# Kernel optimization log

Measured on AMD Instinct MI355X. Metric: run time of the kernel, lower is better.

## Reference

```python
import jax, jax.numpy as jnp
import numpy as np

N, E, F_IN, NUM_GRAPHS, K = 50000, 500000, 160, 128, 3


def _glorot(k, shape):
    lim = np.sqrt(6.0 / (shape[-2] + shape[-1])).astype(np.float32)
    return jax.random.uniform(k, shape, jnp.float32, -lim, lim)


def setup_inputs() -> dict:
    key = jax.random.key(0)
    ks = jax.random.split(key, 8)
    x = jax.random.normal(ks[0], (N, F_IN), jnp.float32)
    edge_index = jax.random.randint(ks[1], (2, E), 0, N)
    edge_attr = jax.random.uniform(ks[2], (E,), jnp.float32)
    batch = jnp.sort(jax.random.randint(ks[3], (N,), 0, NUM_GRAPHS))
    W1 = _glorot(ks[4], (K, F_IN, 128)); b1 = jnp.zeros((128,), jnp.float32)
    W2 = _glorot(ks[5], (K, 128, 64)); b2 = jnp.zeros((64,), jnp.float32)
    W3 = _glorot(ks[6], (K, 64, 32)); b3 = jnp.zeros((32,), jnp.float32)
    Wl = _glorot(ks[7], (32, 2)); bl = jnp.zeros((2,), jnp.float32)
    return dict(x=x, edge_index=edge_index, edge_attr=edge_attr, batch=batch,
                W1=W1, b1=b1, W2=W2, b2=b2, W3=W3, b3=b3, Wl=Wl, bl=bl)


def _cheb_norm(src, dst, edge_attr, n):
    # PyG ChebConv: sym-normalized Laplacian, lambda_max=2 =>
    # L_hat = (2/lmax)*L_sym - I = -D^{-1/2} A D^{-1/2} (diagonal = 0)
    deg = jax.ops.segment_sum(edge_attr, src, num_segments=n)
    safe = jnp.where(deg > 0, deg, 1.0)
    dinv = jnp.where(deg > 0, jax.lax.rsqrt(safe), 0.0)
    return -dinv[src] * edge_attr * dinv[dst]


def _propagate(x, src, dst, w, n):
    # out[dst] += w * x[src]  (sparse L_hat @ x)
    return jax.ops.segment_sum(w[:, None] * x[src], dst, num_segments=n)


def _cheb_conv(x, src, dst, w, W, b, n):
    # Chebyshev recurrence: T0 = x, T1 = L_hat x, Tk = 2 L_hat T(k-1) - T(k-2)
    tx0 = x
    out = tx0 @ W[0]
    tx1 = _propagate(tx0, src, dst, w, n)
    out = out + tx1 @ W[1]
    for k in range(2, W.shape[0]):
        tx2 = 2.0 * _propagate(tx1, src, dst, w, n) - tx0
        out = out + tx2 @ W[k]
        tx0, tx1 = tx1, tx2
    return out + b


def reference(x, edge_index, edge_attr, batch, W1, b1, W2, b2, W3, b3, Wl, bl):
    n = x.shape[0]
    src, dst = edge_index[0], edge_index[1]
    w = _cheb_norm(src, dst, edge_attr, n)
    h = jax.nn.relu(_cheb_conv(x, src, dst, w, W1, b1, n))
    h = jax.nn.relu(_cheb_conv(h, src, dst, w, W2, b2, n))
    h = jax.nn.relu(_cheb_conv(h, src, dst, w, W3, b3, n))
    # global_mean_pool over graph ids (dropout omitted: eval mode)
    sums = jax.ops.segment_sum(h, batch, num_segments=NUM_GRAPHS)
    cnt = jax.ops.segment_sum(jnp.ones((n,), h.dtype), batch, num_segments=NUM_GRAPHS)
    pooled = sums / jnp.maximum(cnt, 1.0)[:, None]
    return pooled @ Wl + bl
```

## Files before the change

kernel.cpp:

```cpp
#include <hip/hip_runtime.h>

#define N_NODES 50000
#define N_EDGES 500000
#define NUM_G   128
#define SCAN_NB 49
#define SCAN_PAD (SCAN_NB * 1024)

typedef __attribute__((ext_vector_type(8))) short short8;
typedef __attribute__((ext_vector_type(4))) float f32x4;

__device__ __forceinline__ unsigned f2bf(float x) {
    unsigned u = __float_as_uint(x);
    return (u + 0x7FFFu + ((u >> 16) & 1u)) >> 16;
}
__device__ __forceinline__ float bf2f(unsigned h) {
    return __uint_as_float(h << 16);
}

__global__ void deg_count_kernel(const int* __restrict__ src, const int* __restrict__ dst,
                                 const float* __restrict__ ea,
                                 float* __restrict__ deg, int* __restrict__ cnt, int E) {
    int e = blockIdx.x * blockDim.x + threadIdx.x;
    if (e < E) {
        atomicAdd(&deg[src[e]], ea[e]);
        atomicAdd(&cnt[dst[e]], 1);
    }
}

__global__ void dinv_kernel(const float* __restrict__ deg, float* __restrict__ dinv, int n) {
    int i = blockIdx.x * blockDim.x + threadIdx.x;
    if (i >= n) return;
    float d = deg[i];
    float r = 0.0f;
    if (d > 0.0f) {
        r = rsqrtf(d);
        r = r * (1.5f - 0.5f * d * r * r);
    }
    dinv[i] = r;
}

__global__ void scan_partial_kernel(const int* __restrict__ cnt, int* __restrict__ partial) {
    int b = blockIdx.x, t = threadIdx.x;
    int4 v = reinterpret_cast<const int4*>(cnt)[b * 256 + t];
    int s = v.x + v.y + v.z + v.w;
    __shared__ int red[256];
    red[t] = s;
    __syncthreads();
    for (int off = 128; off > 0; off >>= 1) {
        if (t < off) red[t] += red[t + off];
        __syncthreads();
    }
    if (t == 0) partial[b] = red[0];
}

__global__ void scan_offsets_kernel(int* __restrict__ partial, int* __restrict__ rowptr,
                                    int nb, int n) {
    int t = threadIdx.x;
    int orig = (t < nb) ? partial[t] : 0;
    int v = orig;
    for (int off = 1; off < 64; off <<= 1) {
        int u = __shfl_up(v, off, 64);
        if (t >= off) v += u;
    }
    if (t < nb) partial[t] = v - orig;
    if (t == nb - 1) rowptr[n] = v;
}

__global__ void scan_final_kernel(const int* __restrict__ cnt, const int* __restrict__ partial,
                                  int* __restrict__ rowptr, int n) {
    int b = blockIdx.x, t = threadIdx.x;
    int4 v = reinterpret_cast<const int4*>(cnt)[b * 256 + t];
    int s = v.x + v.y + v.z + v.w;
    __shared__ int red[256];
    red[t] = s;
    __syncthreads();
    for (int off = 1; off < 256; off <<= 1) {
        int u = (t >= off) ? red[t - off] : 0;
        __syncthreads();
        red[t] += u;
        __syncthreads();
    }
    int excl = partial[b] + ((t == 0) ? 0 : red[t - 1]);
    int i0 = b * 1024 + t * 4;
    if (i0 < n)     rowptr[i0]     = excl;
    if (i0 + 1 < n) rowptr[i0 + 1] = excl + v.x;
    if (i0 + 2 < n) rowptr[i0 + 2] = excl + v.x + v.y;
    if (i0 + 3 < n) rowptr[i0 + 3] = excl + v.x + v.y + v.z;
}

__global__ void scatter_kernel(const int* __restrict__ src, const int* __restrict__ dst,
                               const float* __restrict__ ea, const float* __restrict__ dinv,
                               const int* __restrict__ rowptr, int* __restrict__ fill,
                               int* __restrict__ csr_src, float* __restrict__ csr_w, int E) {
    int e = blockIdx.x * blockDim.x + threadIdx.x;
    if (e >= E) return;
    int s = src[e], d = dst[e];
    float wv = -dinv[s] * ea[e] * dinv[d];
    int pos = rowptr[d] + atomicAdd(&fill[d], 1);
    csr_src[pos] = s;
    csr_w[pos] = wv;
}

__global__ void conv_bf16_kernel(const float* __restrict__ x, unsigned short* __restrict__ o, int n4) {
    int t = blockIdx.x * blockDim.x + threadIdx.x;
    if (t >= n4) return;
    float4 v = reinterpret_cast<const float4*>(x)[t];
    ushort4 r;
    r.x = (unsigned short)f2bf(v.x);
    r.y = (unsigned short)f2bf(v.y);
    r.z = (unsigned short)f2bf(v.z);
    r.w = (unsigned short)f2bf(v.w);
    *reinterpret_cast<ushort4*>(o + (size_t)t * 4) = r;
}

__global__ void wprep_kernel(const float* __restrict__ W, unsigned short* __restrict__ WT,
                             int FIN, int F) {
    int t = blockIdx.x * blockDim.x + threadIdx.x;
    int total = 3 * F * FIN;
    if (t >= total) return;
    int n = t / FIN, k = t - n * FIN;
    int sel = n / F, c = n - sel * F;
    float v;
    if (sel == 0) v = W[(size_t)k * F + c] - W[(size_t)2 * FIN * F + (size_t)k * F + c];
    else          v = W[(size_t)sel * FIN * F + (size_t)k * F + c];
    WT[t] = (unsigned short)f2bf(v);
}

template<int FIN, int F>
__launch_bounds__(256)
__global__ void cheb_gemm(const unsigned short* __restrict__ Xb, const unsigned short* __restrict__ WT,
                          unsigned short* __restrict__ Y0, unsigned short* __restrict__ Y1,
                          unsigned short* __restrict__ Y2,
                          int nrows) {
    constexpr int KT = FIN / 32;
    constexpr int NT = F / 32;
    constexpr int SA = FIN + 8;
    constexpr int F8 = FIN / 8;
    __shared__ short Bs[32 * SA];

    int tid = threadIdx.x;
    int lane = tid & 63, w = tid >> 6;
    int m0 = blockIdx.x * 64;
    int g = blockIdx.y;
    unsigned short* Ys = (g == 0) ? Y0 : (g == 1) ? Y1 : Y2;

    int colb = lane & 15;
    int q8 = (lane >> 4) << 3;
    int rq = (lane >> 4) << 2;
    int arow = m0 + w * 16 + colb;
    bool rok = arow < nrows;

    short8 afr[KT];
    #pragma unroll
    for (int kt = 0; kt < KT; ++kt) {
        short8 z = {0, 0, 0, 0, 0, 0, 0, 0};
        afr[kt] = rok ? *reinterpret_cast<const short8*>(Xb + (size_t)arow * FIN + (kt << 5) + q8) : z;
    }

    for (int nt = 0; nt < NT; ++nt) {
        int n0 = (g * NT + nt) << 5;
        __syncthreads();
        for (int span = tid; span < 32 * F8; span += 256) {
            int r = span / F8, c8 = (span - r * F8) << 3;
            int pr = (r < 16) ? (r << 1) : (((r - 16) << 1) + 1);
            *reinterpret_cast<uint4*>(&Bs[r * SA + c8]) =
                *reinterpret_cast<const uint4*>(WT + (size_t)(n0 + pr) * FIN + c8);
        }
        __syncthreads();

        f32x4 acc0 = {0.f, 0.f, 0.f, 0.f}, acc1 = acc0;
        #pragma unroll
        for (int kt = 0; kt < KT; ++kt) {
            short8 b0 = *reinterpret_cast<const short8*>(&Bs[colb * SA + (kt << 5) + q8]);
            short8 b1 = *reinterpret_cast<const short8*>(&Bs[(colb + 16) * SA + (kt << 5) + q8]);
            acc0 = __builtin_amdgcn_mfma_f32_16x16x32_bf16(afr[kt], b0, acc0, 0, 0, 0);
            acc1 = __builtin_amdgcn_mfma_f32_16x16x32_bf16(afr[kt], b1, acc1, 0, 0, 0);
        }

        int lc = (nt << 5) + (colb << 1);
        #pragma unroll
        for (int r = 0; r < 4; ++r) {
            int orow = m0 + w * 16 + rq + r;
            if (orow < nrows) {
                unsigned pack = f2bf(acc0[r]) | (f2bf(acc1[r]) << 16);
                *reinterpret_cast<unsigned*>(Ys + (size_t)orow * F + lc) = pack;
            }
        }
    }
}

__device__ __forceinline__ void acc8(float* acc, uint4 p, float wv) {
    acc[0] += wv * bf2f(p.x & 0xFFFFu);
    acc[1] += wv * __uint_as_float(p.x & 0xFFFF0000u);
    acc[2] += wv * bf2f(p.y & 0xFFFFu);
    acc[3] += wv * __uint_as_float(p.y & 0xFFFF0000u);
    acc[4] += wv * bf2f(p.z & 0xFFFFu);
    acc[5] += wv * __uint_as_float(p.z & 0xFFFF0000u);
    acc[6] += wv * bf2f(p.w & 0xFFFFu);
    acc[7] += wv * __uint_as_float(p.w & 0xFFFF0000u);
}

__device__ __forceinline__ void expand8(uint4 p, float* o) {
    o[0] = bf2f(p.x & 0xFFFFu);
    o[1] = __uint_as_float(p.x & 0xFFFF0000u);
    o[2] = bf2f(p.y & 0xFFFFu);
    o[3] = __uint_as_float(p.y & 0xFFFF0000u);
    o[4] = bf2f(p.z & 0xFFFFu);
    o[5] = __uint_as_float(p.z & 0xFFFF0000u);
    o[6] = bf2f(p.w & 0xFFFFu);
    o[7] = __uint_as_float(p.w & 0xFFFF0000u);
}

__global__ void gather_z_kernel(const unsigned short* __restrict__ X, const int* __restrict__ csr_src,
                                const float* __restrict__ csr_w, const int* __restrict__ rowptr,
                                const unsigned short* __restrict__ Y1, unsigned short* __restrict__ U,
                                int n, int F) {
    int Fq8 = F >> 3;
    int t = blockIdx.x * blockDim.x + threadIdx.x;
    int d = t / Fq8;
    if (d >= n) return;
    int f8 = (t - d * Fq8) << 3;
    int beg = rowptr[d], end = rowptr[d + 1];
    float acc[8] = {0.f, 0.f, 0.f, 0.f, 0.f, 0.f, 0.f, 0.f};
    int i = beg;
    for (; i + 1 < end; i += 2) {
        int s0 = csr_src[i], s1 = csr_src[i + 1];
        float w0 = csr_w[i], w1 = csr_w[i + 1];
        uint4 p0 = *reinterpret_cast<const uint4*>(X + (size_t)s0 * F + f8);
        uint4 p1 = *reinterpret_cast<const uint4*>(X + (size_t)s1 * F + f8);
        acc8(acc, p0, w0);
        acc8(acc, p1, w1);
    }
    if (i < end) {
        uint4 p0 = *reinterpret_cast<const uint4*>(X + (size_t)csr_src[i] * F + f8);
        acc8(acc, p0, csr_w[i]);
    }
    float y[8];
    expand8(*reinterpret_cast<const uint4*>(Y1 + (size_t)d * F + f8), y);
    uint4 o;
    o.x = f2bf(y[0] + 2.f * acc[0]) | (f2bf(y[1] + 2.f * acc[1]) << 16);
    o.y = f2bf(y[2] + 2.f * acc[2]) | (f2bf(y[3] + 2.f * acc[3]) << 16);
    o.z = f2bf(y[4] + 2.f * acc[4]) | (f2bf(y[5] + 2.f * acc[5]) << 16);
    o.w = f2bf(y[6] + 2.f * acc[6]) | (f2bf(y[7] + 2.f * acc[7]) << 16);
    *reinterpret_cast<uint4*>(U + (size_t)d * F + f8) = o;
}

__global__ void gather_v_kernel(const unsigned short* __restrict__ X, const int* __restrict__ csr_src,
                                const float* __restrict__ csr_w, const int* __restrict__ rowptr,
                                const unsigned short* __restrict__ Y0, const float* __restrict__ bias,
                                unsigned short* __restrict__ Xn, int n, int F) {
    int Fq8 = F >> 3;
    int t = blockIdx.x * blockDim.x + threadIdx.x;
    int d = t / Fq8;
    if (d >= n) return;
    int f8 = (t - d * Fq8) << 3;
    int beg = rowptr[d], end = rowptr[d + 1];
    float acc[8] = {0.f, 0.f, 0.f, 0.f, 0.f, 0.f, 0.f, 0.f};
    int i = beg;
    for (; i + 1 < end; i += 2) {
        int s0 = csr_src[i], s1 = csr_src[i + 1];
        float w0 = csr_w[i], w1 = csr_w[i + 1];
        uint4 p0 = *reinterpret_cast<const uint4*>(X + (size_t)s0 * F + f8);
        uint4 p1 = *reinterpret_cast<const uint4*>(X + (size_t)s1 * F + f8);
        acc8(acc, p0, w0);
        acc8(acc, p1, w1);
    }
    if (i < end) {
        uint4 p0 = *reinterpret_cast<const uint4*>(X + (size_t)csr_src[i] * F + f8);
        acc8(acc, p0, csr_w[i]);
    }
    float y[8];
    expand8(*reinterpret_cast<const uint4*>(Y0 + (size_t)d * F + f8), y);
    float4 ba = *reinterpret_cast<const float4*>(bias + f8);
    float4 bb = *reinterpret_cast<const float4*>(bias + f8 + 4);
    float v0 = fmaxf(y[0] + acc[0] + ba.x, 0.f);
    float v1 = fmaxf(y[1] + acc[1] + ba.y, 0.f);
    float v2 = fmaxf(y[2] + acc[2] + ba.z, 0.f);
    float v3 = fmaxf(y[3] + acc[3] + ba.w, 0.f);
    float v4 = fmaxf(y[4] + acc[4] + bb.x, 0.f);
    float v5 = fmaxf(y[5] + acc[5] + bb.y, 0.f);
    float v6 = fmaxf(y[6] + acc[6] + bb.z, 0.f);
    float v7 = fmaxf(y[7] + acc[7] + bb.w, 0.f);
    uint4 o;
    o.x = f2bf(v0) | (f2bf(v1) << 16);
    o.y = f2bf(v2) | (f2bf(v3) << 16);
    o.z = f2bf(v4) | (f2bf(v5) << 16);
    o.w = f2bf(v6) | (f2bf(v7) << 16);
    *reinterpret_cast<uint4*>(Xn + (size_t)d * F + f8) = o;
}

__device__ __forceinline__ int lower_bound_dev(const int* __restrict__ a, int n, int v) {
    int lo = 0, hi = n;
    while (lo < hi) {
        int mid = (lo + hi) >> 1;
        if (a[mid] < v) lo = mid + 1; else hi = mid;
    }
    return lo;
}

__global__ void pool_kernel(const unsigned short* __restrict__ H, const int* __restrict__ batch,
                            const float* __restrict__ Wl, const float* __restrict__ bl,
                            float* __restrict__ out, int n) {
    int g = blockIdx.x;
    int start = lower_bound_dev(batch, n, g);
    int end   = lower_bound_dev(batch, n, g + 1);
    int tid = threadIdx.x;
    int f = tid & 31;
    int sub = tid >> 5;
    float acc = 0.0f;
    for (int i = start + sub; i < end; i += 8)
        acc += bf2f((unsigned)H[(size_t)i * 32 + f]);
    __shared__ float red[256];
    red[tid] = acc;
    __syncthreads();
    if (tid < 128) red[tid] += red[tid + 128];
    __syncthreads();
    if (tid < 64) red[tid] += red[tid + 64];
    __syncthreads();
    if (tid < 32) red[tid] += red[tid + 32];
    __syncthreads();
    if (tid < 2) {
        int cnt = end - start;
        float inv = 1.0f / (float)(cnt > 0 ? cnt : 1);
        float o = bl[tid];
        for (int f2 = 0; f2 < 32; ++f2)
            o += red[f2] * inv * Wl[f2 * 2 + tid];
        out[g * 2 + tid] = o;
    }
}

extern "C" void kernel_launch(void* const* d_in, const int* in_sizes, int n_in,
                              void* d_out, int out_size, void* d_ws, size_t ws_size,
                              hipStream_t stream) {
    const float* x     = (const float*)d_in[0];
    const int*   ei    = (const int*)d_in[1];
    const float* ea    = (const float*)d_in[2];
    const int*   batch = (const int*)d_in[3];
    const float* W1 = (const float*)d_in[4];
    const float* b1 = (const float*)d_in[5];
    const float* W2 = (const float*)d_in[6];
    const float* b2 = (const float*)d_in[7];
    const float* W3 = (const float*)d_in[8];
    const float* b3 = (const float*)d_in[9];
    const float* Wl = (const float*)d_in[10];
    const float* bl = (const float*)d_in[11];
    float* out = (float*)d_out;
    char* ws = (char*)d_ws;

    const int* src = ei;
    const int* dst = ei + N_EDGES;

    size_t off = 0;
    auto alloc = [&](size_t bytes) { char* p = ws + off; off += (bytes + 255) & ~(size_t)255; return p; };
    float* deg     = (float*)alloc(N_NODES * 4);
    float* dinv    = (float*)alloc(N_NODES * 4);
    int*   cnt     = (int*)  alloc((size_t)SCAN_PAD * 4);
    int*   partial = (int*)  alloc(SCAN_NB * 4);
    int*   rowptr  = (int*)  alloc((N_NODES + 1) * 4);
    int*   fill    = (int*)  alloc(N_NODES * 4);
    int*   csr_src = (int*)  alloc((size_t)N_EDGES * 4);
    float* csr_w   = (float*)alloc((size_t)N_EDGES * 4);
    unsigned short* Xb  = (unsigned short*)alloc((size_t)N_NODES * 160 * 2);
    unsigned short* Y0  = (unsigned short*)alloc((size_t)N_NODES * 128 * 2);
    unsigned short* Y1  = (unsigned short*)alloc((size_t)N_NODES * 128 * 2);
    unsigned short* Y2  = (unsigned short*)alloc((size_t)N_NODES * 128 * 2);
    unsigned short* U   = (unsigned short*)alloc((size_t)N_NODES * 128 * 2);
    unsigned short* WT1 = (unsigned short*)alloc((size_t)384 * 160 * 2);
    unsigned short* WT2 = (unsigned short*)alloc((size_t)192 * 128 * 2);
    unsigned short* WT3 = (unsigned short*)alloc((size_t)96 * 64 * 2);

    const int BT = 256;
    hipMemsetAsync(deg, 0, N_NODES * 4, stream);
    hipMemsetAsync(cnt, 0, (size_t)SCAN_PAD * 4, stream);
    hipMemsetAsync(fill, 0, N_NODES * 4, stream);
    deg_count_kernel<<<(N_EDGES + BT - 1) / BT, BT, 0, stream>>>(src, dst, ea, deg, cnt, N_EDGES);
    dinv_kernel<<<(N_NODES + BT - 1) / BT, BT, 0, stream>>>(deg, dinv, N_NODES);
    scan_partial_kernel<<<SCAN_NB, BT, 0, stream>>>(cnt, partial);
    scan_offsets_kernel<<<1, 64, 0, stream>>>(partial, rowptr, SCAN_NB, N_NODES);
    scan_final_kernel<<<SCAN_NB, BT, 0, stream>>>(cnt, partial, rowptr, N_NODES);
    scatter_kernel<<<(N_EDGES + BT - 1) / BT, BT, 0, stream>>>(src, dst, ea, dinv, rowptr, fill,
                                                               csr_src, csr_w, N_EDGES);
    int n4 = N_NODES * 160 / 4;
    conv_bf16_kernel<<<(n4 + BT - 1) / BT, BT, 0, stream>>>(x, Xb, n4);
    wprep_kernel<<<(3 * 128 * 160 + BT - 1) / BT, BT, 0, stream>>>(W1, WT1, 160, 128);
    wprep_kernel<<<(3 * 64 * 128 + BT - 1) / BT, BT, 0, stream>>>(W2, WT2, 128, 64);
    wprep_kernel<<<(3 * 32 * 64 + BT - 1) / BT, BT, 0, stream>>>(W3, WT3, 64, 32);

    dim3 ggrid((N_NODES + 63) / 64, 3);
    auto gathers = [&](const float* bias, int F) {
        int gth = N_NODES * (F / 8);
        int ggr = (gth + BT - 1) / BT;
        gather_z_kernel<<<ggr, BT, 0, stream>>>(Y2, csr_src, csr_w, rowptr, Y1, U, N_NODES, F);
        gather_v_kernel<<<ggr, BT, 0, stream>>>(U, csr_src, csr_w, rowptr, Y0, bias, Xb, N_NODES, F);
    };

    cheb_gemm<160, 128><<<ggrid, BT, 0, stream>>>(Xb, WT1, Y0, Y1, Y2, N_NODES);
    gathers(b1, 128);
    cheb_gemm<128, 64><<<ggrid, BT, 0, stream>>>(Xb, WT2, Y0, Y1, Y2, N_NODES);
    gathers(b2, 64);
    cheb_gemm<64, 32><<<ggrid, BT, 0, stream>>>(Xb, WT3, Y0, Y1, Y2, N_NODES);
    gathers(b3, 32);

    pool_kernel<<<NUM_G, BT, 0, stream>>>(Xb, batch, Wl, bl, out, N_NODES);
}
```

Baseline: 349.4 us.

## Build CSR with LDS-privatized histograms and per-chunk cursors instead of global atomics

```diff
diff --git a/kernel.cpp b/kernel.cpp
--- a/kernel.cpp
+++ b/kernel.cpp
@@ -4,7 +4,11 @@
 #define N_EDGES 500000
 #define NUM_G   128
 #define SCAN_NB 49
-#define SCAN_PAD (SCAN_NB * 1024)
+#define PN      (SCAN_NB * 1024)
+#define HIST_NCX 25
+#define HIST_EC  20000
+#define HIST_R   8192
+#define HIST_NRY 7
 
 typedef __attribute__((ext_vector_type(8))) short short8;
 typedef __attribute__((ext_vector_type(4))) float f32x4;
@@ -17,26 +21,54 @@
     return __uint_as_float(h << 16);
 }
 
-__global__ void deg_count_kernel(const int* __restrict__ src, const int* __restrict__ dst,
-                                 const float* __restrict__ ea,
-                                 float* __restrict__ deg, int* __restrict__ cnt, int E) {
-    int e = blockIdx.x * blockDim.x + threadIdx.x;
-    if (e < E) {
-        atomicAdd(&deg[src[e]], ea[e]);
-        atomicAdd(&cnt[dst[e]], 1);
-    }
-}
-
-__global__ void dinv_kernel(const float* __restrict__ deg, float* __restrict__ dinv, int n) {
-    int i = blockIdx.x * blockDim.x + threadIdx.x;
-    if (i >= n) return;
-    float d = deg[i];
-    float r = 0.0f;
-    if (d > 0.0f) {
-        r = rsqrtf(d);
-        r = r * (1.5f - 0.5f * d * r * r);
-    }
-    dinv[i] = r;
+__global__ void hist_kernel(const int* __restrict__ src, const int* __restrict__ dst,
+                            const float* __restrict__ ea,
+                            float* __restrict__ pdeg, int* __restrict__ pcnt) {
+    __shared__ float ldeg[HIST_R];
+    __shared__ int   lcnt[HIST_R];
+    int x = blockIdx.x, y = blockIdx.y, tid = threadIdx.x;
+    int base = y * HIST_R;
+    for (int i = tid; i < HIST_R; i += 256) { ldeg[i] = 0.f; lcnt[i] = 0; }
+    __syncthreads();
+    int e0 = x * HIST_EC;
+    for (int e = e0 + tid; e < e0 + HIST_EC; e += 256) {
+        int s = src[e], d = dst[e];
+        float a = ea[e];
+        if ((unsigned)(s - base) < HIST_R) atomicAdd(&ldeg[s - base], a);
+        if ((unsigned)(d - base) < HIST_R) atomicAdd(&lcnt[d - base], 1);
+    }
+    __syncthreads();
+    for (int i = tid; i < HIST_R; i += 256) {
+        int n = base + i;
+        if (n < PN) {
+            pdeg[(size_t)x * PN + n] = ldeg[i];
+            pcnt[(size_t)x * PN + n] = lcnt[i];
+        }
+    }
+}
+
+__global__ void reduce_kernel(float* __restrict__ pdeg, int* __restrict__ pcnt,
+                              float* __restrict__ dinv, int* __restrict__ cnt) {
+    int n = blockIdx.x * 256 + threadIdx.x;
+    float d = 0.f;
+    int run = 0;
+    for (int x = 0; x < HIST_NCX; ++x) {
+        d += pdeg[(size_t)x * PN + n];
+        int v = pcnt[(size_t)x * PN + n];
+        pcnt[(size_t)x * PN + n] = run;
+        run += v;
+    }
+    if (n < N_NODES) {
+        float r = 0.f;
+        if (d > 0.f) {
+            r = rsqrtf(d);
+            r = r * (1.5f - 0.5f * d * r * r);
+        }
+        dinv[n] = r;
+        cnt[n] = run;
+    } else {
+        cnt[n] = 0;
+    }
 }
 
 __global__ void scan_partial_kernel(const int* __restrict__ cnt, int* __restrict__ partial) {
@@ -90,15 +122,27 @@
 
 __global__ void scatter_kernel(const int* __restrict__ src, const int* __restrict__ dst,
                                const float* __restrict__ ea, const float* __restrict__ dinv,
-                               const int* __restrict__ rowptr, int* __restrict__ fill,
-                               int* __restrict__ csr_src, float* __restrict__ csr_w, int E) {
-    int e = blockIdx.x * blockDim.x + threadIdx.x;
-    if (e >= E) return;
-    int s = src[e], d = dst[e];
-    float wv = -dinv[s] * ea[e] * dinv[d];
-    int pos = rowptr[d] + atomicAdd(&fill[d], 1);
-    csr_src[pos] = s;
-    csr_w[pos] = wv;
+                               const int* __restrict__ rowptr, const int* __restrict__ pcnt,
+                               int* __restrict__ csr_src, float* __restrict__ csr_w) {
+    __shared__ int cursor[HIST_R];
+    int x = blockIdx.x, y = blockIdx.y, tid = threadIdx.x;
+    int base = y * HIST_R;
+    for (int i = tid; i < HIST_R; i += 256) {
+        int n = base + i;
+        cursor[i] = (n < N_NODES) ? (rowptr[n] + pcnt[(size_t)x * PN + n]) : 0;
+    }
+    __syncthreads();
+    int e0 = x * HIST_EC;
+    for (int e = e0 + tid; e < e0 + HIST_EC; e += 256) {
+        int d = dst[e];
+        if ((unsigned)(d - base) < HIST_R) {
+            int s = src[e];
+            float wv = -dinv[s] * ea[e] * dinv[d];
+            int pos = atomicAdd(&cursor[d - base], 1);
+            csr_src[pos] = s;
+            csr_w[pos] = wv;
+        }
+    }
 }
 
 __global__ void conv_bf16_kernel(const float* __restrict__ x, unsigned short* __restrict__ o, int n4) {
@@ -113,17 +157,24 @@
     *reinterpret_cast<ushort4*>(o + (size_t)t * 4) = r;
 }
 
-__global__ void wprep_kernel(const float* __restrict__ W, unsigned short* __restrict__ WT,
-                             int FIN, int F) {
-    int t = blockIdx.x * blockDim.x + threadIdx.x;
-    int total = 3 * F * FIN;
-    if (t >= total) return;
+__device__ __forceinline__ void wprep_one(const float* __restrict__ W, unsigned short* __restrict__ WT,
+                                          int t, int FIN, int F) {
     int n = t / FIN, k = t - n * FIN;
     int sel = n / F, c = n - sel * F;
     float v;
     if (sel == 0) v = W[(size_t)k * F + c] - W[(size_t)2 * FIN * F + (size_t)k * F + c];
     else          v = W[(size_t)sel * FIN * F + (size_t)k * F + c];
     WT[t] = (unsigned short)f2bf(v);
+}
+
+__global__ void wprep_all_kernel(const float* __restrict__ W1, const float* __restrict__ W2,
+                                 const float* __restrict__ W3,
+                                 unsigned short* __restrict__ WT1, unsigned short* __restrict__ WT2,
+                                 unsigned short* __restrict__ WT3) {
+    int t = blockIdx.x * 256 + threadIdx.x;
+    if (t < 61440)      wprep_one(W1, WT1, t, 160, 128);
+    else if (t < 86016) wprep_one(W2, WT2, t - 61440, 128, 64);
+    else if (t < 92160) wprep_one(W3, WT3, t - 86016, 64, 32);
 }
 
 template<int FIN, int F>
@@ -352,12 +403,12 @@
 
     size_t off = 0;
     auto alloc = [&](size_t bytes) { char* p = ws + off; off += (bytes + 255) & ~(size_t)255; return p; };
-    float* deg     = (float*)alloc(N_NODES * 4);
+    float* pdeg    = (float*)alloc((size_t)HIST_NCX * PN * 4);
+    int*   pcnt    = (int*)  alloc((size_t)HIST_NCX * PN * 4);
     float* dinv    = (float*)alloc(N_NODES * 4);
-    int*   cnt     = (int*)  alloc((size_t)SCAN_PAD * 4);
+    int*   cnt     = (int*)  alloc((size_t)PN * 4);
     int*   partial = (int*)  alloc(SCAN_NB * 4);
     int*   rowptr  = (int*)  alloc((N_NODES + 1) * 4);
-    int*   fill    = (int*)  alloc(N_NODES * 4);
     int*   csr_src = (int*)  alloc((size_t)N_EDGES * 4);
     float* csr_w   = (float*)alloc((size_t)N_EDGES * 4);
     unsigned short* Xb  = (unsigned short*)alloc((size_t)N_NODES * 160 * 2);
@@ -370,21 +421,18 @@
     unsigned short* WT3 = (unsigned short*)alloc((size_t)96 * 64 * 2);
 
     const int BT = 256;
-    hipMemsetAsync(deg, 0, N_NODES * 4, stream);
-    hipMemsetAsync(cnt, 0, (size_t)SCAN_PAD * 4, stream);
-    hipMemsetAsync(fill, 0, N_NODES * 4, stream);
-    deg_count_kernel<<<(N_EDGES + BT - 1) / BT, BT, 0, stream>>>(src, dst, ea, deg, cnt, N_EDGES);
-    dinv_kernel<<<(N_NODES + BT - 1) / BT, BT, 0, stream>>>(deg, dinv, N_NODES);
+    dim3 hgrid(HIST_NCX, HIST_NRY);
+
+    hist_kernel<<<hgrid, BT, 0, stream>>>(src, dst, ea, pdeg, pcnt);
+    reduce_kernel<<<PN / BT, BT, 0, stream>>>(pdeg, pcnt, dinv, cnt);
     scan_partial_kernel<<<SCAN_NB, BT, 0, stream>>>(cnt, partial);
     scan_offsets_kernel<<<1, 64, 0, stream>>>(partial, rowptr, SCAN_NB, N_NODES);
     scan_final_kernel<<<SCAN_NB, BT, 0, stream>>>(cnt, partial, rowptr, N_NODES);
-    scatter_kernel<<<(N_EDGES + BT - 1) / BT, BT, 0, stream>>>(src, dst, ea, dinv, rowptr, fill,
-                                                               csr_src, csr_w, N_EDGES);
+    scatter_kernel<<<hgrid, BT, 0, stream>>>(src, dst, ea, dinv, rowptr, pcnt, csr_src, csr_w);
+
     int n4 = N_NODES * 160 / 4;
     conv_bf16_kernel<<<(n4 + BT - 1) / BT, BT, 0, stream>>>(x, Xb, n4);
-    wprep_kernel<<<(3 * 128 * 160 + BT - 1) / BT, BT, 0, stream>>>(W1, WT1, 160, 128);
-    wprep_kernel<<<(3 * 64 * 128 + BT - 1) / BT, BT, 0, stream>>>(W2, WT2, 128, 64);
-    wprep_kernel<<<(3 * 32 * 64 + BT - 1) / BT, BT, 0, stream>>>(W3, WT3, 64, 32);
+    wprep_all_kernel<<<360, BT, 0, stream>>>(W1, W2, W3, WT1, WT2, WT3);
 
     dim3 ggrid((N_NODES + 63) / 64, 3);
     auto gathers = [&](const float* bias, int F) {
```

Result: slower. 384.3 us (+10.0%).
